# Optimization experiments

Hardware: AMD Instinct MI355X
Metric: run time of the kernel (lower is better)

Reference implementation:

```python
import jax, jax.numpy as jnp
import numpy as np
from jax import lax

GO = 1  # mead-baseline Offsets.GO
NEG = -10000.0


def setup_inputs() -> dict:
    key = jax.random.key(0)
    k1, k2, k3, k4 = jax.random.split(key, 4)
    B, T, K = 1024, 512, 64
    unary = jax.random.normal(k1, (B, T, K), dtype=jnp.float32)
    lengths = jax.random.randint(k2, (B,), 1, T + 1).astype(jnp.int32)
    inv_mask = jax.random.randint(k3, (K, K), 0, 2).astype(jnp.int32)
    A = (jax.random.normal(k4, (K, K), dtype=jnp.float32) * 0.1)
    return {"unary": unary, "lengths": lengths, "inv_mask": inv_mask, "A": A}


def _viterbi(probv, trans, seq_lens):
    """Masked Viterbi decode (tf.contrib.crf.crf_decode semantics).

    probv: [B, T1, K] unary scores (GO frame already prepended)
    trans: [K, K] transition scores, trans[i, j] = score(i -> j)
    seq_lens: [B] int32, valid lengths (already +1 for the GO frame)
    """
    B, T1, K = probv.shape
    alpha0 = probv[:, 0]                      # [B, K]
    us = jnp.swapaxes(probv[:, 1:], 0, 1)     # [T1-1, B, K]
    ts = jnp.arange(1, T1)

    def fwd(alpha, xs):
        u_t, t = xs
        scores = alpha[:, :, None] + trans[None]        # [B, K_prev, K_cur]
        bp = jnp.argmax(scores, axis=1).astype(jnp.int32)  # [B, K]
        new_alpha = jnp.max(scores, axis=1) + u_t
        alpha = jnp.where((t < seq_lens)[:, None], new_alpha, alpha)  # freeze past length
        return alpha, bp

    alpha_f, bps = lax.scan(fwd, alpha0, (us, ts))  # bps: [T1-1, B, K]
    last = jnp.argmax(alpha_f, axis=-1).astype(jnp.int32)  # [B] tag at last valid step
    best = jnp.max(alpha_f, axis=-1)                       # [B]

    def bwd(tag, xs):
        bp_t, t = xs
        prev = jnp.take_along_axis(bp_t, tag[:, None], axis=1)[:, 0]
        prev = jnp.where(t < seq_lens, prev, tag)  # beyond length: carry tag back
        return prev, prev

    _, prevs = lax.scan(bwd, last, (bps[::-1], ts[::-1]))  # prevs: [T1-1, B] (times T1-2..0)
    tags = jnp.concatenate([prevs[::-1], last[None]], axis=0)  # [T1, B]
    return jnp.swapaxes(tags, 0, 1), best


def reference(unary, lengths, inv_mask, A):
    B, T, K = unary.shape
    inv = inv_mask.astype(jnp.float32) * NEG
    trans = jax.nn.log_softmax(A + inv, axis=-1)
    gos = jnp.full((1, 1, K), NEG, dtype=unary.dtype).at[:, :, GO].set(0.0)
    probv = jnp.concatenate([jnp.broadcast_to(gos, (B, 1, K)), unary], axis=1)  # [B, T+1, K]
    viterbi, _ = _viterbi(probv, trans, lengths.astype(jnp.int32) + 1)
    return viterbi[:, 1:]  # drop GO position -> [B, T]
```

## Files before the change

### kernel.cpp

```cpp
#include <hip/hip_runtime.h>

#define NEGV -10000.0f
#define BB 1024
#define TT 512
#define KK 64

typedef float vf2 __attribute__((ext_vector_type(2)));

__global__ __launch_bounds__(64)
void trans_kernel(const float* __restrict__ A, const int* __restrict__ inv,
                  float* __restrict__ trans)
{
    const int i = blockIdx.x, j = threadIdx.x;
    float x = A[i * KK + j] + (inv[i * KK + j] ? NEGV : 0.0f);
    float m = x;
    #pragma unroll
    for (int o = 32; o > 0; o >>= 1) m = fmaxf(m, __shfl_xor(m, o));
    float e = expf(x - m);
    float s = e;
    #pragma unroll
    for (int o = 32; o > 0; o >>= 1) s += __shfl_xor(s, o);
    trans[i * KK + j] = (x - m) - logf(s);
}

__global__ __launch_bounds__(64, 1)
void viterbi_kernel(const float* __restrict__ unary, const int* __restrict__ lengths,
                    const float* __restrict__ trans, int* __restrict__ out)
{
    const int lane = threadIdx.x;
    const int b = blockIdx.x;

    __shared__ unsigned char sbp[(TT - 1) * KK];
    __shared__ float sAf[2 * KK];

    vf2 Treg2[KK / 2];
    #pragma unroll
    for (int i = 0; i < KK / 2; ++i) {
        Treg2[i].x = trans[(2 * i)     * KK + lane];
        Treg2[i].y = trans[(2 * i + 1) * KK + lane];
    }

    const int len = lengths[b];
    const float* ur = unary + (long)b * (TT * KK);
    int* orow = out + b * TT;

    float uring[8];
    #pragma unroll
    for (int d = 0; d < 8; ++d) uring[d] = ur[d * KK + lane];

    float alpha = (lane == 1) ? 0.0f : NEGV;
    sAf[lane] = alpha;
    __builtin_amdgcn_wave_barrier();

    for (int tb = 1; tb <= len; tb += 8) {
        #pragma unroll
        for (int k = 0; k < 8; ++k) {
            const int t = tb + k;
            const int pin  = k & 1;
            const int pout = (k + 1) & 1;

            const float4* a4p = (const float4*)(sAf + pin * KK);
            float sv[KK];
            #pragma unroll
            for (int i4 = 0; i4 < 16; ++i4) {
                float4 a4 = a4p[i4];
                vf2 t01 = vf2{a4.x, a4.y} + Treg2[2 * i4];
                vf2 t23 = vf2{a4.z, a4.w} + Treg2[2 * i4 + 1];
                sv[4 * i4 + 0] = t01.x; sv[4 * i4 + 1] = t01.y;
                sv[4 * i4 + 2] = t23.x; sv[4 * i4 + 3] = t23.y;
            }

            float l0[22];
            #pragma unroll
            for (int i = 0; i < 21; ++i)
                l0[i] = fmaxf(fmaxf(sv[3 * i], sv[3 * i + 1]), sv[3 * i + 2]);
            l0[21] = sv[63];
            float l1[8];
            #pragma unroll
            for (int i = 0; i < 7; ++i)
                l1[i] = fmaxf(fmaxf(l0[3 * i], l0[3 * i + 1]), l0[3 * i + 2]);
            l1[7] = l0[21];
            float l2a = fmaxf(fmaxf(l1[0], l1[1]), l1[2]);
            float l2b = fmaxf(fmaxf(l1[3], l1[4]), l1[5]);
            float m   = fmaxf(fmaxf(l2a, l2b), fmaxf(l1[6], l1[7]));

            if (t <= len) alpha = m + uring[k];
            sAf[pout * KK + lane] = alpha;
            __builtin_amdgcn_wave_barrier();

            { int rn = t + 7; if (rn > TT - 1) rn = TT - 1;
              uring[k] = ur[rn * KK + lane]; }

            int idx = 63;
            #pragma unroll
            for (int i = 62; i >= 0; --i) idx = (sv[i] == m) ? i : idx;
            if (t >= 2 && t <= len)
                sbp[(t - 2) * KK + lane] = (unsigned char)idx;
        }
    }

    float mm = alpha;
    #pragma unroll
    for (int o = 32; o > 0; o >>= 1) mm = fmaxf(mm, __shfl_xor(mm, o));
    unsigned long long msk = __ballot(alpha == mm);
    int last = __ffsll(msk) - 1;

    for (int jj = len - 1 + lane; jj < TT; jj += 64) orow[jj] = last;

    int tag = last;
    for (int t = len; t >= 2; --t) {
        int prev = sbp[(t - 2) * KK + tag];
        if (lane == 0) orow[t - 2] = prev;
        tag = prev;
    }
}

extern "C" void kernel_launch(void* const* d_in, const int* in_sizes, int n_in,
                              void* d_out, int out_size, void* d_ws, size_t ws_size,
                              hipStream_t stream)
{
    const float* unary   = (const float*)d_in[0];
    const int*   lengths = (const int*)d_in[1];
    const int*   inv     = (const int*)d_in[2];
    const float* A       = (const float*)d_in[3];
    int*         out     = (int*)d_out;

    float* trans = (float*)d_ws;

    trans_kernel<<<KK, KK, 0, stream>>>(A, inv, trans);
    viterbi_kernel<<<BB, KK, 0, stream>>>(unary, lengths, trans, out);
}
```

Measured before the change: 505.0 us.

## Broadcast alpha via readlane instead of LDS round-trip; double-buffer unary prefetch

Result: slower. 635.2 us (+25.8%).

```diff
diff --git a/kernel.cpp b/kernel.cpp
--- a/kernel.cpp
+++ b/kernel.cpp
@@ -4,8 +4,6 @@
 #define BB 1024
 #define TT 512
 #define KK 64
-
-typedef float vf2 __attribute__((ext_vector_type(2)));
 
 __global__ __launch_bounds__(64)
 void trans_kernel(const float* __restrict__ A, const int* __restrict__ inv,
@@ -23,6 +21,48 @@
     trans[i * KK + j] = (x - m) - logf(s);
 }
 
+
+#define FILL4(BUF_, RB_)                                                       \
+  { _Pragma("unroll")                                                          \
+    for (int d_ = 0; d_ < 4; ++d_) {                                           \
+        int r_ = (RB_) + d_; if (r_ > TT - 1) r_ = TT - 1;                     \
+        BUF_[d_] = ur[r_ * KK + lane];                                         \
+    } }
+
+#define STEP(T_, UV_)                                                          \
+  {                                                                            \
+    float sv[KK];                                                              \
+    _Pragma("unroll")                                                          \
+    for (int i = 0; i < KK; ++i) {                                             \
+        int rl_ = __builtin_amdgcn_readlane(__float_as_int(alpha), i);         \
+        sv[i] = __int_as_float(rl_) + Treg[i];                                 \
+    }                                                                          \
+    float u_ = (UV_);                                                          \
+    asm volatile("" : "+v"(u_));   \
+        \
+    float l0[22];                                                              \
+    _Pragma("unroll")                                                          \
+    for (int i = 0; i < 21; ++i)                                               \
+        l0[i] = fmaxf(fmaxf(sv[3 * i], sv[3 * i + 1]), sv[3 * i + 2]);         \
+    l0[21] = sv[63];                                                           \
+    float l1[8];                                                               \
+    _Pragma("unroll")                                                          \
+    for (int i = 0; i < 7; ++i)                                                \
+        l1[i] = fmaxf(fmaxf(l0[3 * i], l0[3 * i + 1]), l0[3 * i + 2]);         \
+    l1[7] = l0[21];                                                            \
+    float l2a = fmaxf(fmaxf(l1[0], l1[1]), l1[2]);                             \
+    float l2b = fmaxf(fmaxf(l1[3], l1[4]), l1[5]);                             \
+    float m_  = fmaxf(fmaxf(l2a, l2b), fmaxf(l1[6], l1[7]));                   \
+      \
+    if ((T_) <= len) alpha = m_ + u_;                                          \
+      \
+    int idx = 63;                                                              \
+    _Pragma("unroll")                                                          \
+    for (int i = 62; i >= 0; --i) idx = (sv[i] == m_) ? i : idx;               \
+    if ((T_) >= 2 && (T_) <= len)                                              \
+        sbp[((T_) - 2) * KK + lane] = (unsigned char)idx;                      \
+  }
+
 __global__ __launch_bounds__(64, 1)
 void viterbi_kernel(const float* __restrict__ unary, const int* __restrict__ lengths,
                     const float* __restrict__ trans, int* __restrict__ out)
@@ -31,72 +71,28 @@
     const int b = blockIdx.x;
 
     __shared__ unsigned char sbp[(TT - 1) * KK];
-    __shared__ float sAf[2 * KK];
 
-    vf2 Treg2[KK / 2];
+    float Treg[KK];
     #pragma unroll
-    for (int i = 0; i < KK / 2; ++i) {
-        Treg2[i].x = trans[(2 * i)     * KK + lane];
-        Treg2[i].y = trans[(2 * i + 1) * KK + lane];
-    }
+    for (int i = 0; i < KK; ++i) Treg[i] = trans[i * KK + lane];
 
     const int len = lengths[b];
     const float* ur = unary + (long)b * (TT * KK);
     int* orow = out + b * TT;
 
-    float uring[8];
-    #pragma unroll
-    for (int d = 0; d < 8; ++d) uring[d] = ur[d * KK + lane];
+    float ub0[4], ub1[4];
+    FILL4(ub0, 0)
+    FILL4(ub1, 4)
 
     float alpha = (lane == 1) ? 0.0f : NEGV;
-    sAf[lane] = alpha;
-    __builtin_amdgcn_wave_barrier();
 
     for (int tb = 1; tb <= len; tb += 8) {
-        #pragma unroll
-        for (int k = 0; k < 8; ++k) {
-            const int t = tb + k;
-            const int pin  = k & 1;
-            const int pout = (k + 1) & 1;
-
-            const float4* a4p = (const float4*)(sAf + pin * KK);
-            float sv[KK];
-            #pragma unroll
-            for (int i4 = 0; i4 < 16; ++i4) {
-                float4 a4 = a4p[i4];
-                vf2 t01 = vf2{a4.x, a4.y} + Treg2[2 * i4];
-                vf2 t23 = vf2{a4.z, a4.w} + Treg2[2 * i4 + 1];
-                sv[4 * i4 + 0] = t01.x; sv[4 * i4 + 1] = t01.y;
-                sv[4 * i4 + 2] = t23.x; sv[4 * i4 + 3] = t23.y;
-            }
-
-            float l0[22];
-            #pragma unroll
-            for (int i = 0; i < 21; ++i)
-                l0[i] = fmaxf(fmaxf(sv[3 * i], sv[3 * i + 1]), sv[3 * i + 2]);
-            l0[21] = sv[63];
-            float l1[8];
-            #pragma unroll
-            for (int i = 0; i < 7; ++i)
-                l1[i] = fmaxf(fmaxf(l0[3 * i], l0[3 * i + 1]), l0[3 * i + 2]);
-            l1[7] = l0[21];
-            float l2a = fmaxf(fmaxf(l1[0], l1[1]), l1[2]);
-            float l2b = fmaxf(fmaxf(l1[3], l1[4]), l1[5]);
-            float m   = fmaxf(fmaxf(l2a, l2b), fmaxf(l1[6], l1[7]));
-
-            if (t <= len) alpha = m + uring[k];
-            sAf[pout * KK + lane] = alpha;
-            __builtin_amdgcn_wave_barrier();
-
-            { int rn = t + 7; if (rn > TT - 1) rn = TT - 1;
-              uring[k] = ur[rn * KK + lane]; }
-
-            int idx = 63;
-            #pragma unroll
-            for (int i = 62; i >= 0; --i) idx = (sv[i] == m) ? i : idx;
-            if (t >= 2 && t <= len)
-                sbp[(t - 2) * KK + lane] = (unsigned char)idx;
-        }
+        STEP(tb + 0, ub0[0]) STEP(tb + 1, ub0[1])
+        STEP(tb + 2, ub0[2]) STEP(tb + 3, ub0[3])
+        FILL4(ub0, tb + 7)
+        STEP(tb + 4, ub1[0]) STEP(tb + 5, ub1[1])
+        STEP(tb + 6, ub1[2]) STEP(tb + 7, ub1[3])
+        FILL4(ub1, tb + 11)
     }
 
     float mm = alpha;
@@ -106,6 +102,8 @@
     int last = __ffsll(msk) - 1;
 
     for (int jj = len - 1 + lane; jj < TT; jj += 64) orow[jj] = last;
+
+    __builtin_amdgcn_s_waitcnt(0);
 
     int tag = last;
     for (int t = len; t >= 2; --t) {
```
